# Optimization experiments

Measured on AMD Instinct MI355X. Metric: run time of the kernel, lower is better.

The kernel has to match this reference:

```python
import jax, jax.numpy as jnp
import numpy as np

B, N, D = 4, 4096, 1024
H = 16
DH = D // H  # 64
SCALE = DH ** 0.5


def setup_inputs() -> dict:
    key = jax.random.key(0)
    ks = jax.random.split(key, 10)
    bound = float(np.sqrt(6.0 / (D + D)))  # xavier_uniform for square weights
    lin_b = float(1.0 / np.sqrt(D))        # default nn.Linear bias init bound
    return {
        "q": jax.random.normal(ks[0], (B, N, D), dtype=jnp.float32),
        "k": jax.random.normal(ks[1], (B, N, D), dtype=jnp.float32),
        "v": jax.random.normal(ks[2], (B, N, D), dtype=jnp.float32),
        "Wq": jax.random.uniform(ks[3], (D, D), jnp.float32, -bound, bound),
        "bq": jax.random.uniform(ks[4], (D,), jnp.float32, -lin_b, lin_b),
        "Wk": jax.random.uniform(ks[5], (D, D), jnp.float32, -bound, bound),
        "bk": jax.random.uniform(ks[6], (D,), jnp.float32, -lin_b, lin_b),
        "Wv": jax.random.uniform(ks[7], (D, D), jnp.float32, -bound, bound),
        "bv": jax.random.uniform(ks[8], (D,), jnp.float32, -lin_b, lin_b),
        "Wo": jax.random.uniform(ks[9], (D, D), jnp.float32, -bound, bound),
    }


def _split_heads(x):
    # [b, n, h*d] -> [b, h, n, d]
    b, n, _ = x.shape
    return x.reshape(b, n, H, DH).transpose(0, 2, 1, 3)


def reference(q, k, v, Wq, bq, Wk, bk, Wv, bv, Wo):
    qp = _split_heads(q @ Wq.T + bq)  # [b,h,n,d]
    kp = _split_heads(k @ Wk.T + bk)
    vp = _split_heads(v @ Wv.T + bv)

    inv_qtr = SCALE ** (-0.25)
    qs = jax.nn.softmax(qp, axis=-1) * inv_qtr            # feature-wise softmax on Q
    ctx = jnp.einsum('bhnd,bhne->bhde', kp, vp)           # K^T V: [b,h,d,d]
    ctx = jax.nn.softmax(ctx, axis=-2) * inv_qtr          # softmax over first d axis
    att = jnp.einsum('bhnd,bhde->bhne', qs, ctx)          # [b,h,n,d]

    att = att.transpose(0, 2, 1, 3).reshape(q.shape[0], q.shape[1], D)  # b n (h d)
    return att @ Wo.T  # to_out linear (no bias); dropout p=0 -> identity
```

## Files before the change

### kernel.cpp

```cpp
#include <hip/hip_runtime.h>

#define INV_QTR 0.59460355750136053f

typedef _Float16 f16;
typedef _Float16 f16x8 __attribute__((ext_vector_type(8)));
typedef float f32x4 __attribute__((ext_vector_type(4)));

__device__ __forceinline__ void gload16(const void* g, void* l) {
    __builtin_amdgcn_global_load_lds(
        (const __attribute__((address_space(1))) void*)g,
        (__attribute__((address_space(3))) void*)l, 16, 0, 0);
}

template <bool OF, bool BIAS, bool QSM>
__device__ __forceinline__ void gemm_f16_body(const f16* __restrict__ X,
                                              const f16* __restrict__ W,
                                              const float* __restrict__ bias,
                                              void* __restrict__ dst) {
    __shared__ __align__(16) f16 As[128 * 64];
    __shared__ __align__(16) f16 Bs[128 * 64];

    const int tid  = threadIdx.x;
    const int lane = tid & 63;
    const int wave = tid >> 6;
    const int m0   = blockIdx.x * 128;
    const int n0   = blockIdx.y * 128;
    const int wm   = (wave >> 1) * 64;
    const int wn   = (wave & 1) * 64;
    const int frow = lane & 15;
    const int quad = lane >> 4;

    f32x4 acc[4][4] = {};

    for (int k0 = 0; k0 < 1024; k0 += 64) {
        __syncthreads();
        #pragma unroll
        for (int i = 0; i < 4; ++i) {
            int slot = i * 256 + tid;
            int row  = slot >> 3;
            int sc   = slot & 7;
            int gc   = sc ^ (row & 7);
            gload16(X + (size_t)(m0 + row) * 1024 + k0 + gc * 8,
                    (char*)As + slot * 16);
            gload16(W + (size_t)(n0 + row) * 1024 + k0 + gc * 8,
                    (char*)Bs + slot * 16);
        }
        __syncthreads();

        #pragma unroll
        for (int kk = 0; kk < 2; ++kk) {
            f16x8 fa[4], fb[4];
            #pragma unroll
            for (int t = 0; t < 4; ++t) {
                int arow = wm + t * 16 + frow;
                int asc  = (kk * 4 + quad) ^ (arow & 7);
                fa[t] = *(const f16x8*)(As + arow * 64 + asc * 8);
                int brow = wn + t * 16 + frow;
                int bsc  = (kk * 4 + quad) ^ (brow & 7);
                fb[t] = *(const f16x8*)(Bs + brow * 64 + bsc * 8);
            }
            #pragma unroll
            for (int tm = 0; tm < 4; ++tm)
                #pragma unroll
                for (int tn = 0; tn < 4; ++tn)
                    acc[tm][tn] = __builtin_amdgcn_mfma_f32_16x16x32_f16(
                        fa[tm], fb[tn], acc[tm][tn], 0, 0, 0);
        }
    }

    if (QSM) {
        float badd[4];
        #pragma unroll
        for (int tn = 0; tn < 4; ++tn) badd[tn] = bias[n0 + wn + tn * 16 + frow];
        #pragma unroll
        for (int tm = 0; tm < 4; ++tm) {
            #pragma unroll
            for (int r = 0; r < 4; ++r) {
                float x[4], m = -1e30f;
                #pragma unroll
                for (int tn = 0; tn < 4; ++tn) {
                    x[tn] = acc[tm][tn][r] + badd[tn];
                    m = fmaxf(m, x[tn]);
                }
                #pragma unroll
                for (int s = 1; s < 16; s <<= 1) m = fmaxf(m, __shfl_xor(m, s, 64));
                float e[4], sum = 0.f;
                #pragma unroll
                for (int tn = 0; tn < 4; ++tn) { e[tn] = __expf(x[tn] - m); sum += e[tn]; }
                #pragma unroll
                for (int s = 1; s < 16; s <<= 1) sum += __shfl_xor(sum, s, 64);
                float inv = INV_QTR / sum;
                size_t rowb = (size_t)(m0 + wm + tm * 16 + quad * 4 + r) * 1024;
                #pragma unroll
                for (int tn = 0; tn < 4; ++tn)
                    ((f16*)dst)[rowb + n0 + wn + tn * 16 + frow] = (f16)(e[tn] * inv);
            }
        }
        return;
    }

    #pragma unroll
    for (int tn = 0; tn < 4; ++tn) {
        int col = n0 + wn + tn * 16 + frow;
        float badd = BIAS ? bias[col] : 0.0f;
        #pragma unroll
        for (int tm = 0; tm < 4; ++tm) {
            #pragma unroll
            for (int r = 0; r < 4; ++r) {
                size_t idx = (size_t)(m0 + wm + tm * 16 + quad * 4 + r) * 1024 + col;
                float v = acc[tm][tn][r] + badd;
                if (OF) ((float*)dst)[idx] = v;
                else    ((f16*)dst)[idx] = (f16)v;
            }
        }
    }
}

__global__ void proj_qsm_gemm(const f16* __restrict__ X, const f16* __restrict__ W,
                              const float* __restrict__ bias, f16* __restrict__ dst) {
    gemm_f16_body<false, true, true>(X, W, bias, dst);
}

__global__ void out_gemm(const f16* __restrict__ att, const f16* __restrict__ Wo,
                         float* __restrict__ out) {
    gemm_f16_body<true, false, false>(att, Wo, nullptr, out);
}

template <int MODE, bool CS>
__global__ void transpose_cvt(const float* __restrict__ src, f16* __restrict__ dst0,
                              f16* __restrict__ dst1, float* __restrict__ csum) {
    __shared__ float T[64][65];
    int n0 = blockIdx.x * 64, c0 = blockIdx.y * 64, b = blockIdx.z;
    int tid = threadIdx.x;
    const float* s = src + ((size_t)b * 4096 + n0) * 1024 + c0;
    int r = tid >> 2, q4 = tid & 3;
    #pragma unroll
    for (int i = 0; i < 4; ++i) {
        f32x4 v = *(const f32x4*)(s + (size_t)r * 1024 + q4 * 16 + i * 4);
        #pragma unroll
        for (int j = 0; j < 4; ++j) T[q4 * 16 + i * 4 + j][r] = v[j];
    }
    __syncthreads();
    int cc = tid >> 2, nq = tid & 3;
    size_t obase = ((size_t)b * 1024 + c0 + cc) * 4096 + n0 + nq * 16;
    float x[16];
    #pragma unroll
    for (int j = 0; j < 16; ++j) x[j] = T[cc][nq * 16 + j];
    if (CS) {
        float ssum = 0.f;
        #pragma unroll
        for (int j = 0; j < 16; ++j) ssum += x[j];
        ssum += __shfl_xor(ssum, 1, 64);
        ssum += __shfl_xor(ssum, 2, 64);
        if (nq == 0) atomicAdd(csum + b * 1024 + c0 + cc, ssum);
    }
    f16x8 hi0, hi1;
    #pragma unroll
    for (int j = 0; j < 8; ++j) { hi0[j] = (f16)x[j]; hi1[j] = (f16)x[8 + j]; }
    if (MODE == 0 || MODE == 1) {
        *(f16x8*)(dst0 + obase) = hi0;
        *(f16x8*)(dst0 + obase + 8) = hi1;
    }
    if (MODE == 0 || MODE == 2) {
        f16x8 lo0, lo1;
        #pragma unroll
        for (int j = 0; j < 8; ++j) {
            lo0[j] = (f16)(x[j] - (float)hi0[j]);
            lo1[j] = (f16)(x[8 + j] - (float)hi1[j]);
        }
        f16* d = (MODE == 0) ? dst1 : dst0;
        *(f16x8*)(d + obase) = lo0;
        *(f16x8*)(d + obase + 8) = lo1;
    }
}

template <int NB, bool ACCUM>
__global__ void gram_gemm(const f16* __restrict__ A, const f16* __restrict__ B0,
                          const f16* __restrict__ B1, float* __restrict__ G0,
                          float* __restrict__ G1) {
    __shared__ __align__(16) f16 As[128 * 64];
    __shared__ __align__(16) f16 Bs0[128 * 64];
    __shared__ __align__(16) f16 Bs1[NB == 2 ? 128 * 64 : 8];
    const int tid = threadIdx.x, lane = tid & 63, wave = tid >> 6;
    const int zsel = blockIdx.x;
    const int m0 = blockIdx.y * 128, n0 = blockIdx.z * 128;
    const int b = zsel >> 1, kh = zsel & 1;
    const int wm = (wave >> 1) * 64, wn = (wave & 1) * 64;
    const int frow = lane & 15, quad = lane >> 4;
    const f16* Ab  = A + (size_t)b * 4194304;
    const f16* B0b = B0 + (size_t)b * 4194304;
    const f16* B1b = (NB == 2) ? B1 + (size_t)b * 4194304 : nullptr;
    float* Gd = (kh ? G1 : G0) + (size_t)b * 1048576;
    const int kbase = kh * 2048;
    f32x4 acc[4][4] = {};

    for (int k0 = kbase; k0 < kbase + 2048; k0 += 64) {
        __syncthreads();
        #pragma unroll
        for (int i = 0; i < 4; ++i) {
            int slot = i * 256 + tid, row = slot >> 3, sc = slot & 7;
            int gc = sc ^ (row & 7);
            gload16(Ab + (size_t)(m0 + row) * 4096 + k0 + gc * 8, (char*)As + slot * 16);
            gload16(B0b + (size_t)(n0 + row) * 4096 + k0 + gc * 8, (char*)Bs0 + slot * 16);
            if (NB == 2)
                gload16(B1b + (size_t)(n0 + row) * 4096 + k0 + gc * 8, (char*)Bs1 + slot * 16);
        }
        __syncthreads();
        #pragma unroll
        for (int kk = 0; kk < 2; ++kk) {
            f16x8 fa[4], fb0[4], fb1[4];
            #pragma unroll
            for (int t = 0; t < 4; ++t) {
                int arow = wm + t * 16 + frow;
                int asc  = (kk * 4 + quad) ^ (arow & 7);
                fa[t] = *(const f16x8*)(As + arow * 64 + asc * 8);
                int brow = wn + t * 16 + frow;
                int bsc  = (kk * 4 + quad) ^ (brow & 7);
                fb0[t] = *(const f16x8*)(Bs0 + brow * 64 + bsc * 8);
                if (NB == 2) fb1[t] = *(const f16x8*)(Bs1 + brow * 64 + bsc * 8);
            }
            #pragma unroll
            for (int tm = 0; tm < 4; ++tm)
                #pragma unroll
                for (int tn = 0; tn < 4; ++tn) {
                    acc[tm][tn] = __builtin_amdgcn_mfma_f32_16x16x32_f16(
                        fa[tm], fb0[tn], acc[tm][tn], 0, 0, 0);
                    if (NB == 2)
                        acc[tm][tn] = __builtin_amdgcn_mfma_f32_16x16x32_f16(
                            fa[tm], fb1[tn], acc[tm][tn], 0, 0, 0);
                }
        }
    }
    #pragma unroll
    for (int tn = 0; tn < 4; ++tn) {
        int col = n0 + wn + tn * 16 + frow;
        #pragma unroll
        for (int tm = 0; tm < 4; ++tm)
            #pragma unroll
            for (int r = 0; r < 4; ++r) {
                size_t idx = (size_t)(m0 + wm + tm * 16 + quad * 4 + r) * 1024 + col;
                if (ACCUM) Gd[idx] += acc[tm][tn][r];
                else       Gd[idx]  = acc[tm][tn][r];
            }
    }
}

__global__ void combine_split(const float* __restrict__ a, const float* __restrict__ b,
                              f16* __restrict__ hi, f16* __restrict__ lo) {
    size_t i = ((size_t)blockIdx.x * 256 + threadIdx.x) * 8;
    f32x4 a0 = *(const f32x4*)(a + i);
    f32x4 a1 = *(const f32x4*)(a + i + 4);
    f32x4 b0 = *(const f32x4*)(b + i);
    f32x4 b1 = *(const f32x4*)(b + i + 4);
    f16x8 h, l;
    #pragma unroll
    for (int j = 0; j < 4; ++j) {
        float s0 = a0[j] + b0[j], s1 = a1[j] + b1[j];
        h[j] = (f16)s0;     l[j] = (f16)(s0 - (float)h[j]);
        h[4 + j] = (f16)s1; l[4 + j] = (f16)(s1 - (float)h[4 + j]);
    }
    *(f16x8*)(hi + i) = h;
    *(f16x8*)(lo + i) = l;
}

__global__ void a3f16_gemm(const f16* __restrict__ wkhi, const f16* __restrict__ wklo,
                           const f16* __restrict__ ghi, const f16* __restrict__ glo,
                           float* __restrict__ P0, float* __restrict__ P1) {
    __shared__ __align__(16) f16 As0[128 * 64], As1[128 * 64];
    __shared__ __align__(16) f16 Bs0[128 * 64], Bs1[128 * 64];
    const int tid = threadIdx.x, lane = tid & 63, wave = tid >> 6;
    const int zsel = blockIdx.x;
    const int m0 = blockIdx.y * 128, n0 = blockIdx.z * 128;
    const int b = zsel >> 1, kh = zsel & 1;
    const int wm = (wave >> 1) * 64, wn = (wave & 1) * 64;
    const int frow = lane & 15, quad = lane >> 4;
    const f16* g0b = ghi + (size_t)b * 1048576;
    const f16* g1b = glo + (size_t)b * 1048576;
    float* Pd = (kh ? P1 : P0) + (size_t)b * 1048576;
    const int kbase = kh * 512;
    f32x4 acc[4][4] = {};

    for (int k0 = kbase; k0 < kbase + 512; k0 += 64) {
        __syncthreads();
        #pragma unroll
        for (int i = 0; i < 4; ++i) {
            int slot = i * 256 + tid, row = slot >> 3, sc = slot & 7;
            int gc = sc ^ (row & 7);
            size_t ao = (size_t)(m0 + row) * 1024 + k0 + gc * 8;
            size_t bo = (size_t)(n0 + row) * 1024 + k0 + gc * 8;
            gload16(wkhi + ao, (char*)As0 + slot * 16);
            gload16(wklo + ao, (char*)As1 + slot * 16);
            gload16(g0b + bo, (char*)Bs0 + slot * 16);
            gload16(g1b + bo, (char*)Bs1 + slot * 16);
        }
        __syncthreads();
        #pragma unroll
        for (int kk = 0; kk < 2; ++kk) {
            f16x8 fa0[4], fa1[4], fb0[4], fb1[4];
            #pragma unroll
            for (int t = 0; t < 4; ++t) {
                int arow = wm + t * 16 + frow;
                int asc  = (kk * 4 + quad) ^ (arow & 7);
                fa0[t] = *(const f16x8*)(As0 + arow * 64 + asc * 8);
                fa1[t] = *(const f16x8*)(As1 + arow * 64 + asc * 8);
                int brow = wn + t * 16 + frow;
                int bsc  = (kk * 4 + quad) ^ (brow & 7);
                fb0[t] = *(const f16x8*)(Bs0 + brow * 64 + bsc * 8);
                fb1[t] = *(const f16x8*)(Bs1 + brow * 64 + bsc * 8);
            }
            #pragma unroll
            for (int tm = 0; tm < 4; ++tm)
                #pragma unroll
                for (int tn = 0; tn < 4; ++tn) {
                    acc[tm][tn] = __builtin_amdgcn_mfma_f32_16x16x32_f16(
                        fa0[tm], fb0[tn], acc[tm][tn], 0, 0, 0);
                    acc[tm][tn] = __builtin_amdgcn_mfma_f32_16x16x32_f16(
                        fa1[tm], fb0[tn], acc[tm][tn], 0, 0, 0);
                    acc[tm][tn] = __builtin_amdgcn_mfma_f32_16x16x32_f16(
                        fa0[tm], fb1[tn], acc[tm][tn], 0, 0, 0);
                }
        }
    }
    #pragma unroll
    for (int tn = 0; tn < 4; ++tn) {
        int col = n0 + wn + tn * 16 + frow;
        #pragma unroll
        for (int tm = 0; tm < 4; ++tm)
            #pragma unroll
            for (int r = 0; r < 4; ++r)
                Pd[(size_t)(m0 + wm + tm * 16 + quad * 4 + r) * 1024 + col] =
                    acc[tm][tn][r];
    }
}

__global__ void zero_f32(float* __restrict__ p) {
    size_t i = ((size_t)blockIdx.x * 256 + threadIdx.x) * 4;
    *(f32x4*)(p + i) = f32x4{0.f, 0.f, 0.f, 0.f};
}

__global__ void bias_vec(const float* __restrict__ sk, const float* __restrict__ sv,
                         const float* __restrict__ Wk, const float* __restrict__ Wv,
                         float* __restrict__ u, float* __restrict__ w) {
    int gid = blockIdx.x * 4 + (threadIdx.x >> 6);
    int lane = threadIdx.x & 63;
    int b = gid >> 10, d = gid & 1023;
    const float* W = blockIdx.y ? Wv : Wk;
    const float* s = blockIdx.y ? sv : sk;
    float* dst = blockIdx.y ? w : u;
    const float* wr = W + (size_t)d * 1024;
    const float* sr = s + b * 1024;
    float acc = 0.f;
    #pragma unroll
    for (int t = 0; t < 16; ++t) acc += wr[lane + t * 64] * sr[lane + t * 64];
    #pragma unroll
    for (int s2 = 32; s2; s2 >>= 1) acc += __shfl_xor(acc, s2, 64);
    if (lane == 0) dst[b * 1024 + d] = acc;
}

__global__ void ctx_gemm_softmax(const f16* __restrict__ a3hi, const f16* __restrict__ a3lo,
                                 const f16* __restrict__ wvhi, const f16* __restrict__ wvlo,
                                 const float* __restrict__ u, const float* __restrict__ wvec,
                                 const float* __restrict__ bk, const float* __restrict__ bv,
                                 f16* __restrict__ ctxT) {
    __shared__ __align__(16) f16 As0[64 * 64], As1[64 * 64], Bs0[64 * 64], Bs1[64 * 64];
    __shared__ float cs[64 * 65];
    int bh = blockIdx.x, b = bh >> 4, h = bh & 15;
    int tid = threadIdx.x, lane = tid & 63, wave = tid >> 6;
    const size_t abase = (size_t)b * 1048576 + (size_t)(h * 64) * 1024;
    const size_t wbase = (size_t)(h * 64) * 1024;
    int frow = lane & 15, quad = lane >> 4;
    f32x4 acc[4] = {};

    for (int k0 = 0; k0 < 1024; k0 += 64) {
        __syncthreads();
        #pragma unroll
        for (int i = 0; i < 2; ++i) {
            int slot = i * 256 + tid, row = slot >> 3, sc = slot & 7;
            int gc = sc ^ (row & 7);
            size_t ro = (size_t)row * 1024 + k0 + gc * 8;
            gload16(a3hi + abase + ro, (char*)As0 + slot * 16);
            gload16(a3lo + abase + ro, (char*)As1 + slot * 16);
            gload16(wvhi + wbase + ro, (char*)Bs0 + slot * 16);
            gload16(wvlo + wbase + ro, (char*)Bs1 + slot * 16);
        }
        __syncthreads();
        #pragma unroll
        for (int kk = 0; kk < 2; ++kk) {
            int arow = wave * 16 + frow;
            int asc  = (kk * 4 + quad) ^ (arow & 7);
            f16x8 fa0 = *(const f16x8*)(As0 + arow * 64 + asc * 8);
            f16x8 fa1 = *(const f16x8*)(As1 + arow * 64 + asc * 8);
            #pragma unroll
            for (int tn = 0; tn < 4; ++tn) {
                int brow = tn * 16 + frow;
                int bsc  = (kk * 4 + quad) ^ (brow & 7);
                f16x8 fb0 = *(const f16x8*)(Bs0 + brow * 64 + bsc * 8);
                f16x8 fb1 = *(const f16x8*)(Bs1 + brow * 64 + bsc * 8);
                acc[tn] = __builtin_amdgcn_mfma_f32_16x16x32_f16(fa0, fb0, acc[tn], 0, 0, 0);
                acc[tn] = __builtin_amdgcn_mfma_f32_16x16x32_f16(fa1, fb0, acc[tn], 0, 0, 0);
                acc[tn] = __builtin_amdgcn_mfma_f32_16x16x32_f16(fa0, fb1, acc[tn], 0, 0, 0);
            }
        }
    }

    const float* ub  = u + b * 1024 + h * 64;
    const float* wb  = wvec + b * 1024 + h * 64;
    const float* bkh = bk + h * 64;
    const float* bvh = bv + h * 64;
    #pragma unroll
    for (int tn = 0; tn < 4; ++tn) {
        int ee = tn * 16 + frow;
        float bve = bvh[ee], we = wb[ee];
        #pragma unroll
        for (int r = 0; r < 4; ++r) {
            int dd = wave * 16 + quad * 4 + r;
            float bkd = bkh[dd], ud = ub[dd];
            cs[dd * 65 + ee] = acc[tn][r] + bkd * we + bve * ud + 4096.0f * bkd * bve;
        }
    }
    __syncthreads();
    #pragma unroll
    for (int i = 0; i < 16; ++i) {
        int e = wave * 16 + i;
        float x = cs[lane * 65 + e];
        float m = x;
        #pragma unroll
        for (int s2 = 32; s2; s2 >>= 1) m = fmaxf(m, __shfl_xor(m, s2, 64));
        float ex = __expf(x - m);
        float sum = ex;
        #pragma unroll
        for (int s2 = 32; s2; s2 >>= 1) sum += __shfl_xor(sum, s2, 64);
        ctxT[((size_t)bh * 64 + e) * 64 + lane] = (f16)(ex / sum * INV_QTR);
    }
}

__global__ void att_gemm(const f16* __restrict__ qs, const f16* __restrict__ ctxT,
                         f16* __restrict__ att) {
    __shared__ __align__(16) f16 As[2][128 * 64];
    __shared__ __align__(16) f16 Bs[2][64 * 64];
    int tid = threadIdx.x, lane = tid & 63, wave = tid >> 6;
    int m0 = blockIdx.x * 128;
    int n0 = blockIdx.y * 128;
    int b  = m0 >> 12;
    int h0 = (n0 >> 6) & 15;

    #pragma unroll
    for (int ch = 0; ch < 2; ++ch) {
        #pragma unroll
        for (int i = 0; i < 4; ++i) {
            int slot = i * 256 + tid, row = slot >> 3, sc = slot & 7, gc = sc ^ (row & 7);
            gload16(qs + (size_t)(m0 + row) * 1024 + n0 + ch * 64 + gc * 8,
                    (char*)As[ch] + slot * 16);
        }
        #pragma unroll
        for (int i = 0; i < 2; ++i) {
            int slot = i * 256 + tid, row = slot >> 3, sc = slot & 7, gc = sc ^ (row & 7);
            int bh = b * 16 + h0 + ch;
            gload16(ctxT + ((size_t)bh * 64 + row) * 64 + gc * 8,
                    (char*)Bs[ch] + slot * 16);
        }
    }
    __syncthreads();

    int wm = (wave >> 1) * 64, wn = wave & 1;
    int frow = lane & 15, quad = lane >> 4;
    f32x4 acc[4][4] = {};
    #pragma unroll
    for (int kk = 0; kk < 2; ++kk) {
        f16x8 fa[4], fb[4];
        #pragma unroll
        for (int t = 0; t < 4; ++t) {
            int arow = wm + t * 16 + frow;
            int asc  = (kk * 4 + quad) ^ (arow & 7);
            fa[t] = *(const f16x8*)(As[wn] + arow * 64 + asc * 8);
            int brow = t * 16 + frow;
            int bsc  = (kk * 4 + quad) ^ (brow & 7);
            fb[t] = *(const f16x8*)(Bs[wn] + brow * 64 + bsc * 8);
        }
        #pragma unroll
        for (int tm = 0; tm < 4; ++tm)
            #pragma unroll
            for (int tn = 0; tn < 4; ++tn)
                acc[tm][tn] = __builtin_amdgcn_mfma_f32_16x16x32_f16(
                    fa[tm], fb[tn], acc[tm][tn], 0, 0, 0);
    }
    #pragma unroll
    for (int tn = 0; tn < 4; ++tn) {
        int col = n0 + wn * 64 + tn * 16 + frow;
        #pragma unroll
        for (int tm = 0; tm < 4; ++tm) {
            #pragma unroll
            for (int r = 0; r < 4; ++r) {
                int row = m0 + wm + tm * 16 + quad * 4 + r;
                att[(size_t)row * 1024 + col] = (f16)acc[tm][tn][r];
            }
        }
    }
}

__device__ __forceinline__ void cvt8_hilo(const float* src, f16* dh, f16* dl, bool lo) {
    f32x4 a = ((const f32x4*)src)[0];
    f32x4 b = ((const f32x4*)src)[1];
    f16x8 h, l;
    #pragma unroll
    for (int j = 0; j < 4; ++j) {
        h[j] = (f16)a[j];     h[j + 4] = (f16)b[j];
        l[j] = (f16)(a[j] - (float)h[j]);
        l[j + 4] = (f16)(b[j] - (float)h[j + 4]);
    }
    *(f16x8*)dh = h;
    if (lo) *(f16x8*)dl = l;
}

__global__ void cvt_w_kv(const float* __restrict__ Wk, const float* __restrict__ Wv,
                         f16* __restrict__ whik, f16* __restrict__ whiv,
                         f16* __restrict__ wlok, f16* __restrict__ wlov) {
    const float* s = blockIdx.y ? Wv : Wk;
    f16* dh = blockIdx.y ? whiv : whik;
    f16* dl = blockIdx.y ? wlov : wlok;
    size_t i = ((size_t)blockIdx.x * 256 + threadIdx.x) * 8;
    cvt8_hilo(s + i, dh + i, dl + i, true);
}

__global__ void cvt_q_wqo(const float* __restrict__ q, const float* __restrict__ Wq,
                          const float* __restrict__ Wo, f16* __restrict__ qh,
                          f16* __restrict__ wqhi, f16* __restrict__ wohi) {
    size_t i = ((size_t)blockIdx.x * 256 + threadIdx.x) * 8;
    const float* src;
    f16* dst;
    if (i < 16777216) { src = q + i; dst = qh + i; }
    else {
        size_t wi = i - 16777216;
        if (wi < 1048576) { src = Wq + wi; dst = wqhi + wi; }
        else              { src = Wo + (wi - 1048576); dst = wohi + (wi - 1048576); }
    }
    cvt8_hilo(src, dst, nullptr, false);
}

extern "C" void kernel_launch(void* const* d_in, const int* in_sizes, int n_in,
                              void* d_out, int out_size, void* d_ws, size_t ws_size,
                              hipStream_t stream) {
    const float* q  = (const float*)d_in[0];
    const float* k  = (const float*)d_in[1];
    const float* v  = (const float*)d_in[2];
    const float* Wq = (const float*)d_in[3];
    const float* bq = (const float*)d_in[4];
    const float* Wk = (const float*)d_in[5];
    const float* bk = (const float*)d_in[6];
    const float* Wv = (const float*)d_in[7];
    const float* bv = (const float*)d_in[8];
    const float* Wo = (const float*)d_in[9];

    const size_t Mi = 1048576;
    char* ws = (char*)d_ws;
    char* ob = (char*)d_out;

    f16*   Ghi  = (f16*)ws;
    f16*   Glo  = (f16*)(ws + 8 * Mi);
    f16*   A3hi = (f16*)(ws + 16 * Mi);
    f16*   A3lo = (f16*)(ws + 24 * Mi);
    float* G0   = (float*)(ws + 32 * Mi);
    float* G1   = (float*)(ws + 48 * Mi);
    f16*   Wkhi = (f16*)(ws + 64 * Mi);
    f16*   Wvhi = (f16*)(ws + 66 * Mi);
    f16*   Wklo = (f16*)(ws + 68 * Mi);
    f16*   Wvlo = (f16*)(ws + 70 * Mi);
    f16*   ctxT = (f16*)(ws + 72 * Mi);
    float* sk   = (float*)(ws + 72 * Mi + 524288);
    float* sv   = (float*)(ws + 72 * Mi + 540672);
    float* u    = (float*)(ws + 72 * Mi + 557056);
    float* w    = (float*)(ws + 72 * Mi + 573440);
    f16*   XvTh = (f16*)ws;
    f16*   Wqhi = (f16*)(ws + 32 * Mi);
    f16*   Wohi = (f16*)(ws + 34 * Mi);
    f16*   att  = (f16*)(ws + 36 * Mi);

    f16*   XkTh = (f16*)ob;
    f16*   XkTl = (f16*)(ob + 32 * Mi);
    f16*   XvTl = (f16*)(ob + 32 * Mi);
    float* P0   = (float*)ob;
    float* P1   = (float*)(ob + 16 * Mi);
    f16*   qh   = (f16*)ob;
    f16*   qp   = (f16*)(ob + 32 * Mi);
    float* out  = (float*)d_out;

    zero_f32<<<8, 256, 0, stream>>>(sk);
    cvt_w_kv<<<dim3(512, 2), 256, 0, stream>>>(Wk, Wv, Wkhi, Wvhi, Wklo, Wvlo);
    transpose_cvt<0, true><<<dim3(64, 16, 4), 256, 0, stream>>>(k, XkTh, XkTl, sk);
    transpose_cvt<1, true><<<dim3(64, 16, 4), 256, 0, stream>>>(v, XvTh, nullptr, sv);
    gram_gemm<2, false><<<dim3(8, 8, 8), 256, 0, stream>>>(XvTh, XkTh, XkTl, G0, G1);
    transpose_cvt<2, false><<<dim3(64, 16, 4), 256, 0, stream>>>(v, XvTl, nullptr, nullptr);
    gram_gemm<1, true><<<dim3(8, 8, 8), 256, 0, stream>>>(XvTl, XkTh, nullptr, G0, G1);
    combine_split<<<2048, 256, 0, stream>>>(G0, G1, Ghi, Glo);
    a3f16_gemm<<<dim3(8, 8, 8), 256, 0, stream>>>(Wkhi, Wklo, Ghi, Glo, P0, P1);
    combine_split<<<2048, 256, 0, stream>>>(P0, P1, A3hi, A3lo);
    bias_vec<<<dim3(1024, 2), 256, 0, stream>>>(sk, sv, Wk, Wv, u, w);
    ctx_gemm_softmax<<<64, 256, 0, stream>>>(A3hi, A3lo, Wvhi, Wvlo, u, w, bk, bv, ctxT);
    cvt_q_wqo<<<9216, 256, 0, stream>>>(q, Wq, Wo, qh, Wqhi, Wohi);
    proj_qsm_gemm<<<dim3(128, 8), 256, 0, stream>>>(qh, Wqhi, bq, qp);
    att_gemm<<<dim3(128, 8), 256, 0, stream>>>(qp, ctxT, att);
    out_gemm<<<dim3(128, 8), 256, 0, stream>>>(att, Wohi, out);
}
```

Baseline: 597.1 us.

## Fuse Q projection softmax with attention GEMM and merge small prep kernels

Fuses the Q projection, its feature-wise softmax, and the qs·ctx product into one kernel that keeps the softmaxed tile in shared memory, so the qp intermediate is never written to or read from global memory. It also merges the weight conversion with the K/V transposes, and the bias-vector computation with the G combine. The column sums now use per-block partial writes plus a reduction in place of atomics and a zeroing kernel. The P0+P1 combine and hi/lo split is folded into the ctx kernel's tile loads. Together these cut launch count and intermediate global traffic, at the cost of more shared memory per block and register pressure in the fused kernel.

```diff
diff --git a/kernel.cpp b/kernel.cpp
--- a/kernel.cpp
+++ b/kernel.cpp
@@ -12,7 +12,7 @@
         (__attribute__((address_space(3))) void*)l, 16, 0, 0);
 }
 
-template <bool OF, bool BIAS, bool QSM>
+template <bool OF, bool BIAS>
 __device__ __forceinline__ void gemm_f16_body(const f16* __restrict__ X,
                                               const f16* __restrict__ W,
                                               const float* __restrict__ bias,
@@ -68,37 +68,6 @@
         }
     }
 
-    if (QSM) {
-        float badd[4];
-        #pragma unroll
-        for (int tn = 0; tn < 4; ++tn) badd[tn] = bias[n0 + wn + tn * 16 + frow];
-        #pragma unroll
-        for (int tm = 0; tm < 4; ++tm) {
-            #pragma unroll
-            for (int r = 0; r < 4; ++r) {
-                float x[4], m = -1e30f;
-                #pragma unroll
-                for (int tn = 0; tn < 4; ++tn) {
-                    x[tn] = acc[tm][tn][r] + badd[tn];
-                    m = fmaxf(m, x[tn]);
-                }
-                #pragma unroll
-                for (int s = 1; s < 16; s <<= 1) m = fmaxf(m, __shfl_xor(m, s, 64));
-                float e[4], sum = 0.f;
-                #pragma unroll
-                for (int tn = 0; tn < 4; ++tn) { e[tn] = __expf(x[tn] - m); sum += e[tn]; }
-                #pragma unroll
-                for (int s = 1; s < 16; s <<= 1) sum += __shfl_xor(sum, s, 64);
-                float inv = INV_QTR / sum;
-                size_t rowb = (size_t)(m0 + wm + tm * 16 + quad * 4 + r) * 1024;
-                #pragma unroll
-                for (int tn = 0; tn < 4; ++tn)
-                    ((f16*)dst)[rowb + n0 + wn + tn * 16 + frow] = (f16)(e[tn] * inv);
-            }
-        }
-        return;
-    }
-
     #pragma unroll
     for (int tn = 0; tn < 4; ++tn) {
         int col = n0 + wn + tn * 16 + frow;
@@ -116,21 +85,19 @@
     }
 }
 
-__global__ void proj_qsm_gemm(const f16* __restrict__ X, const f16* __restrict__ W,
-                              const float* __restrict__ bias, f16* __restrict__ dst) {
-    gemm_f16_body<false, true, true>(X, W, bias, dst);
-}
-
 __global__ void out_gemm(const f16* __restrict__ att, const f16* __restrict__ Wo,
                          float* __restrict__ out) {
-    gemm_f16_body<true, false, false>(att, Wo, nullptr, out);
+    gemm_f16_body<true, false>(att, Wo, nullptr, out);
 }
 
 template <int MODE, bool CS>
-__global__ void transpose_cvt(const float* __restrict__ src, f16* __restrict__ dst0,
-                              f16* __restrict__ dst1, float* __restrict__ csum) {
-    __shared__ float T[64][65];
-    int n0 = blockIdx.x * 64, c0 = blockIdx.y * 64, b = blockIdx.z;
+__device__ __forceinline__ void transpose_body(const float* __restrict__ src,
+                                               f16* __restrict__ dst0,
+                                               f16* __restrict__ dst1,
+                                               float* __restrict__ csum,
+                                               int bx, int by, int bz,
+                                               float (*T)[65]) {
+    int n0 = bx * 64, c0 = by * 64, b = bz;
     int tid = threadIdx.x;
     const float* s = src + ((size_t)b * 4096 + n0) * 1024 + c0;
     int r = tid >> 2, q4 = tid & 3;
@@ -152,7 +119,7 @@
         for (int j = 0; j < 16; ++j) ssum += x[j];
         ssum += __shfl_xor(ssum, 1, 64);
         ssum += __shfl_xor(ssum, 2, 64);
-        if (nq == 0) atomicAdd(csum + b * 1024 + c0 + cc, ssum);
+        if (nq == 0) csum[((size_t)(b * 1024 + c0 + cc)) * 64 + bx] = ssum;
     }
     f16x8 hi0, hi1;
     #pragma unroll
@@ -171,6 +138,66 @@
         f16* d = (MODE == 0) ? dst1 : dst0;
         *(f16x8*)(d + obase) = lo0;
         *(f16x8*)(d + obase + 8) = lo1;
+    }
+}
+
+__device__ __forceinline__ void cvt8_hilo(const float* src, f16* dh, f16* dl, bool lo) {
+    f32x4 a = ((const f32x4*)src)[0];
+    f32x4 b = ((const f32x4*)src)[1];
+    f16x8 h, l;
+    #pragma unroll
+    for (int j = 0; j < 4; ++j) {
+        h[j] = (f16)a[j];     h[j + 4] = (f16)b[j];
+        l[j] = (f16)(a[j] - (float)h[j]);
+        l[j + 4] = (f16)(b[j] - (float)h[j + 4]);
+    }
+    *(f16x8*)dh = h;
+    if (lo) *(f16x8*)dl = l;
+}
+
+__global__ void prep_kernel(const float* __restrict__ k, const float* __restrict__ v,
+                            const float* __restrict__ Wk, const float* __restrict__ Wv,
+                            f16* __restrict__ XkTh, f16* __restrict__ XkTl,
+                            f16* __restrict__ XvTh,
+                            f16* __restrict__ whik, f16* __restrict__ whiv,
+                            f16* __restrict__ wlok, f16* __restrict__ wlov,
+                            float* __restrict__ pk, float* __restrict__ pv) {
+    __shared__ float T[64][65];
+    int bid = blockIdx.x;
+    if (bid < 4096) {
+        transpose_body<0, true>(k, XkTh, XkTl, pk, bid & 63, (bid >> 6) & 15,
+                                bid >> 10, T);
+    } else if (bid < 8192) {
+        int g = bid - 4096;
+        transpose_body<1, true>(v, XvTh, nullptr, pv, g & 63, (g >> 6) & 15,
+                                g >> 10, T);
+    } else {
+        int g = bid - 8192;
+        const float* s = (g >= 512) ? Wv : Wk;
+        f16* dh = (g >= 512) ? whiv : whik;
+        f16* dl = (g >= 512) ? wlov : wlok;
+        size_t i = ((size_t)(g & 511) * 256 + threadIdx.x) * 8;
+        cvt8_hilo(s + i, dh + i, dl + i, true);
+    }
+}
+
+__global__ void tvlo_kernel(const float* __restrict__ v, f16* __restrict__ XvTl,
+                            const float* __restrict__ pk, const float* __restrict__ pv,
+                            float* __restrict__ sk, float* __restrict__ sv) {
+    __shared__ float T[64][65];
+    int bid = blockIdx.x;
+    if (bid < 4096) {
+        transpose_body<2, false>(v, XvTl, nullptr, nullptr, bid & 63,
+                                 (bid >> 6) & 15, bid >> 10, T);
+    } else {
+        int idx = (bid - 4096) * 256 + threadIdx.x;
+        const float* p = (idx < 4096) ? pk : pv;
+        float* d = (idx < 4096) ? sk : sv;
+        int c = idx & 4095;
+        float s = 0.f;
+        #pragma unroll
+        for (int ch = 0; ch < 64; ++ch) s += p[(size_t)c * 64 + ch];
+        d[c] = s;
     }
 }
 
@@ -245,22 +272,45 @@
     }
 }
 
-__global__ void combine_split(const float* __restrict__ a, const float* __restrict__ b,
-                              f16* __restrict__ hi, f16* __restrict__ lo) {
-    size_t i = ((size_t)blockIdx.x * 256 + threadIdx.x) * 8;
-    f32x4 a0 = *(const f32x4*)(a + i);
-    f32x4 a1 = *(const f32x4*)(a + i + 4);
-    f32x4 b0 = *(const f32x4*)(b + i);
-    f32x4 b1 = *(const f32x4*)(b + i + 4);
-    f16x8 h, l;
-    #pragma unroll
-    for (int j = 0; j < 4; ++j) {
-        float s0 = a0[j] + b0[j], s1 = a1[j] + b1[j];
-        h[j] = (f16)s0;     l[j] = (f16)(s0 - (float)h[j]);
-        h[4 + j] = (f16)s1; l[4 + j] = (f16)(s1 - (float)h[4 + j]);
-    }
-    *(f16x8*)(hi + i) = h;
-    *(f16x8*)(lo + i) = l;
+__global__ void mid_kernel(const float* __restrict__ G0, const float* __restrict__ G1,
+                           f16* __restrict__ Ghi, f16* __restrict__ Glo,
+                           const float* __restrict__ sk, const float* __restrict__ sv,
+                           const float* __restrict__ Wk, const float* __restrict__ Wv,
+                           float* __restrict__ u, float* __restrict__ w) {
+    int bid = blockIdx.x;
+    if (bid < 2048) {
+        size_t i = ((size_t)bid * 256 + threadIdx.x) * 8;
+        f32x4 a0 = *(const f32x4*)(G0 + i);
+        f32x4 a1 = *(const f32x4*)(G0 + i + 4);
+        f32x4 b0 = *(const f32x4*)(G1 + i);
+        f32x4 b1 = *(const f32x4*)(G1 + i + 4);
+        f16x8 h, l;
+        #pragma unroll
+        for (int j = 0; j < 4; ++j) {
+            float s0 = a0[j] + b0[j], s1 = a1[j] + b1[j];
+            h[j] = (f16)s0;     l[j] = (f16)(s0 - (float)h[j]);
+            h[4 + j] = (f16)s1; l[4 + j] = (f16)(s1 - (float)h[4 + j]);
+        }
+        *(f16x8*)(Ghi + i) = h;
+        *(f16x8*)(Glo + i) = l;
+    } else {
+        int g = bid - 2048;
+        int yy = g >> 10;
+        int gid = (g & 1023) * 4 + (threadIdx.x >> 6);
+        int lane = threadIdx.x & 63;
+        int b = gid >> 10, d = gid & 1023;
+        const float* W = yy ? Wv : Wk;
+        const float* s = yy ? sv : sk;
+        float* dst = yy ? w : u;
+        const float* wr = W + (size_t)d * 1024;
+        const float* sr = s + b * 1024;
+        float acc = 0.f;
+        #pragma unroll
+        for (int t = 0; t < 16; ++t) acc += wr[lane + t * 64] * sr[lane + t * 64];
+        #pragma unroll
+        for (int s2 = 32; s2; s2 >>= 1) acc += __shfl_xor(acc, s2, 64);
+        if (lane == 0) dst[b * 1024 + d] = acc;
+    }
 }
 
 __global__ void a3f16_gemm(const f16* __restrict__ wkhi, const f16* __restrict__ wklo,
@@ -333,40 +383,17 @@
     }
 }
 
-__global__ void zero_f32(float* __restrict__ p) {
-    size_t i = ((size_t)blockIdx.x * 256 + threadIdx.x) * 4;
-    *(f32x4*)(p + i) = f32x4{0.f, 0.f, 0.f, 0.f};
-}
-
-__global__ void bias_vec(const float* __restrict__ sk, const float* __restrict__ sv,
-                         const float* __restrict__ Wk, const float* __restrict__ Wv,
-                         float* __restrict__ u, float* __restrict__ w) {
-    int gid = blockIdx.x * 4 + (threadIdx.x >> 6);
-    int lane = threadIdx.x & 63;
-    int b = gid >> 10, d = gid & 1023;
-    const float* W = blockIdx.y ? Wv : Wk;
-    const float* s = blockIdx.y ? sv : sk;
-    float* dst = blockIdx.y ? w : u;
-    const float* wr = W + (size_t)d * 1024;
-    const float* sr = s + b * 1024;
-    float acc = 0.f;
-    #pragma unroll
-    for (int t = 0; t < 16; ++t) acc += wr[lane + t * 64] * sr[lane + t * 64];
-    #pragma unroll
-    for (int s2 = 32; s2; s2 >>= 1) acc += __shfl_xor(acc, s2, 64);
-    if (lane == 0) dst[b * 1024 + d] = acc;
-}
-
-__global__ void ctx_gemm_softmax(const f16* __restrict__ a3hi, const f16* __restrict__ a3lo,
-                                 const f16* __restrict__ wvhi, const f16* __restrict__ wvlo,
-                                 const float* __restrict__ u, const float* __restrict__ wvec,
-                                 const float* __restrict__ bk, const float* __restrict__ bv,
-                                 f16* __restrict__ ctxT) {
+__global__ void ctx_ps(const float* __restrict__ P0, const float* __restrict__ P1,
+                       const f16* __restrict__ wvhi, const f16* __restrict__ wvlo,
+                       const float* __restrict__ u, const float* __restrict__ wvec,
+                       const float* __restrict__ bk, const float* __restrict__ bv,
+                       f16* __restrict__ ctxT) {
     __shared__ __align__(16) f16 As0[64 * 64], As1[64 * 64], Bs0[64 * 64], Bs1[64 * 64];
     __shared__ float cs[64 * 65];
     int bh = blockIdx.x, b = bh >> 4, h = bh & 15;
     int tid = threadIdx.x, lane = tid & 63, wave = tid >> 6;
-    const size_t abase = (size_t)b * 1048576 + (size_t)(h * 64) * 1024;
+    const float* p0b = P0 + (size_t)b * 1048576 + (size_t)(h * 64) * 1024;
+    const float* p1b = P1 + (size_t)b * 1048576 + (size_t)(h * 64) * 1024;
     const size_t wbase = (size_t)(h * 64) * 1024;
     int frow = lane & 15, quad = lane >> 4;
     f32x4 acc[4] = {};
@@ -378,8 +405,19 @@
             int slot = i * 256 + tid, row = slot >> 3, sc = slot & 7;
             int gc = sc ^ (row & 7);
             size_t ro = (size_t)row * 1024 + k0 + gc * 8;
-            gload16(a3hi + abase + ro, (char*)As0 + slot * 16);
-            gload16(a3lo + abase + ro, (char*)As1 + slot * 16);
+            f32x4 xa = *(const f32x4*)(p0b + ro);
+            f32x4 xb = *(const f32x4*)(p0b + ro + 4);
+            f32x4 ya = *(const f32x4*)(p1b + ro);
+            f32x4 yb = *(const f32x4*)(p1b + ro + 4);
+            f16x8 hh, ll;
+            #pragma unroll
+            for (int j = 0; j < 4; ++j) {
+                float s0 = xa[j] + ya[j], s1 = xb[j] + yb[j];
+                hh[j] = (f16)s0;     ll[j] = (f16)(s0 - (float)hh[j]);
+                hh[4 + j] = (f16)s1; ll[4 + j] = (f16)(s1 - (float)hh[4 + j]);
+            }
+            *(f16x8*)((char*)As0 + slot * 16) = hh;
+            *(f16x8*)((char*)As1 + slot * 16) = ll;
             gload16(wvhi + wbase + ro, (char*)Bs0 + slot * 16);
             gload16(wvlo + wbase + ro, (char*)Bs1 + slot * 16);
         }
@@ -432,94 +470,6 @@
         for (int s2 = 32; s2; s2 >>= 1) sum += __shfl_xor(sum, s2, 64);
         ctxT[((size_t)bh * 64 + e) * 64 + lane] = (f16)(ex / sum * INV_QTR);
     }
-}
-
-__global__ void att_gemm(const f16* __restrict__ qs, const f16* __restrict__ ctxT,
-                         f16* __restrict__ att) {
-    __shared__ __align__(16) f16 As[2][128 * 64];
-    __shared__ __align__(16) f16 Bs[2][64 * 64];
-    int tid = threadIdx.x, lane = tid & 63, wave = tid >> 6;
-    int m0 = blockIdx.x * 128;
-    int n0 = blockIdx.y * 128;
-    int b  = m0 >> 12;
-    int h0 = (n0 >> 6) & 15;
-
-    #pragma unroll
-    for (int ch = 0; ch < 2; ++ch) {
-        #pragma unroll
-        for (int i = 0; i < 4; ++i) {
-            int slot = i * 256 + tid, row = slot >> 3, sc = slot & 7, gc = sc ^ (row & 7);
-            gload16(qs + (size_t)(m0 + row) * 1024 + n0 + ch * 64 + gc * 8,
-                    (char*)As[ch] + slot * 16);
-        }
-        #pragma unroll
-        for (int i = 0; i < 2; ++i) {
-            int slot = i * 256 + tid, row = slot >> 3, sc = slot & 7, gc = sc ^ (row & 7);
-            int bh = b * 16 + h0 + ch;
-            gload16(ctxT + ((size_t)bh * 64 + row) * 64 + gc * 8,
-                    (char*)Bs[ch] + slot * 16);
-        }
-    }
-    __syncthreads();
-
-    int wm = (wave >> 1) * 64, wn = wave & 1;
-    int frow = lane & 15, quad = lane >> 4;
-    f32x4 acc[4][4] = {};
-    #pragma unroll
-    for (int kk = 0; kk < 2; ++kk) {
-        f16x8 fa[4], fb[4];
-        #pragma unroll
-        for (int t = 0; t < 4; ++t) {
-            int arow = wm + t * 16 + frow;
-            int asc  = (kk * 4 + quad) ^ (arow & 7);
-            fa[t] = *(const f16x8*)(As[wn] + arow * 64 + asc * 8);
-            int brow = t * 16 + frow;
-            int bsc  = (kk * 4 + quad) ^ (brow & 7);
-            fb[t] = *(const f16x8*)(Bs[wn] + brow * 64 + bsc * 8);
-        }
-        #pragma unroll
-        for (int tm = 0; tm < 4; ++tm)
-            #pragma unroll
-            for (int tn = 0; tn < 4; ++tn)
-                acc[tm][tn] = __builtin_amdgcn_mfma_f32_16x16x32_f16(
-                    fa[tm], fb[tn], acc[tm][tn], 0, 0, 0);
-    }
-    #pragma unroll
-    for (int tn = 0; tn < 4; ++tn) {
-        int col = n0 + wn * 64 + tn * 16 + frow;
-        #pragma unroll
-        for (int tm = 0; tm < 4; ++tm) {
-            #pragma unroll
-            for (int r = 0; r < 4; ++r) {
-                int row = m0 + wm + tm * 16 + quad * 4 + r;
-                att[(size_t)row * 1024 + col] = (f16)acc[tm][tn][r];
-            }
-        }
-    }
-}
-
-__device__ __forceinline__ void cvt8_hilo(const float* src, f16* dh, f16* dl, bool lo) {
-    f32x4 a = ((const f32x4*)src)[0];
-    f32x4 b = ((const f32x4*)src)[1];
-    f16x8 h, l;
-    #pragma unroll
-    for (int j = 0; j < 4; ++j) {
-        h[j] = (f16)a[j];     h[j + 4] = (f16)b[j];
-        l[j] = (f16)(a[j] - (float)h[j]);
-        l[j + 4] = (f16)(b[j] - (float)h[j + 4]);
-    }
-    *(f16x8*)dh = h;
-    if (lo) *(f16x8*)dl = l;
-}
-
-__global__ void cvt_w_kv(const float* __restrict__ Wk, const float* __restrict__ Wv,
-                         f16* __restrict__ whik, f16* __restrict__ whiv,
-                         f16* __restrict__ wlok, f16* __restrict__ wlov) {
-    const float* s = blockIdx.y ? Wv : Wk;
-    f16* dh = blockIdx.y ? whiv : whik;
-    f16* dl = blockIdx.y ? wlov : wlok;
-    size_t i = ((size_t)blockIdx.x * 256 + threadIdx.x) * 8;
-    cvt8_hilo(s + i, dh + i, dl + i, true);
 }
 
 __global__ void cvt_q_wqo(const float* __restrict__ q, const float* __restrict__ Wq,
@@ -535,6 +485,136 @@
         else              { src = Wo + (wi - 1048576); dst = wohi + (wi - 1048576); }
     }
     cvt8_hilo(src, dst, nullptr, false);
+}
+
+__global__ void __launch_bounds__(256)
+proj_att(const f16* __restrict__ qh, const f16* __restrict__ Wqhi,
+         const float* __restrict__ bias, const f16* __restrict__ ctxT,
+         f16* __restrict__ att) {
+    __shared__ __align__(16) char SMEM[34816];
+    __shared__ __align__(16) f16 ctxS[2][4096];
+    f16* As  = (f16*)SMEM;
+    f16* Bs  = (f16*)(SMEM + 16384);
+    f16* qsS = (f16*)SMEM;
+
+    const int tid  = threadIdx.x;
+    const int lane = tid & 63;
+    const int wave = tid >> 6;
+    const int m0   = blockIdx.x * 128;
+    const int n0   = blockIdx.y * 128;
+    const int wm   = (wave >> 1) * 64;
+    const int wn   = (wave & 1) * 64;
+    const int frow = lane & 15;
+    const int quad = lane >> 4;
+    const int b    = m0 >> 12;
+    const int h0   = (n0 >> 6) & 15;
+
+    #pragma unroll
+    for (int ch = 0; ch < 2; ++ch)
+        #pragma unroll
+        for (int i = 0; i < 2; ++i) {
+            int slot = i * 256 + tid, row = slot >> 3, gc = (slot & 7) ^ (row & 7);
+            int bh = b * 16 + h0 + ch;
+            gload16(ctxT + ((size_t)bh * 64 + row) * 64 + gc * 8,
+                    (char*)ctxS[ch] + slot * 16);
+        }
+
+    f32x4 acc[4][4] = {};
+    for (int k0 = 0; k0 < 1024; k0 += 64) {
+        __syncthreads();
+        #pragma unroll
+        for (int i = 0; i < 4; ++i) {
+            int slot = i * 256 + tid, row = slot >> 3, sc = slot & 7;
+            int gc = sc ^ (row & 7);
+            gload16(qh + (size_t)(m0 + row) * 1024 + k0 + gc * 8,
+                    (char*)As + slot * 16);
+            gload16(Wqhi + (size_t)(n0 + row) * 1024 + k0 + gc * 8,
+                    (char*)Bs + slot * 16);
+        }
+        __syncthreads();
+        #pragma unroll
+        for (int kk = 0; kk < 2; ++kk) {
+            f16x8 fa[4], fb[4];
+            #pragma unroll
+            for (int t = 0; t < 4; ++t) {
+                int arow = wm + t * 16 + frow;
+                int asc  = (kk * 4 + quad) ^ (arow & 7);
+                fa[t] = *(const f16x8*)(As + arow * 64 + asc * 8);
+                int brow = wn + t * 16 + frow;
+                int bsc  = (kk * 4 + quad) ^ (brow & 7);
+                fb[t] = *(const f16x8*)(Bs + brow * 64 + bsc * 8);
+            }
+            #pragma unroll
+            for (int tm = 0; tm < 4; ++tm)
+                #pragma unroll
+                for (int tn = 0; tn < 4; ++tn)
+                    acc[tm][tn] = __builtin_amdgcn_mfma_f32_16x16x32_f16(
+                        fa[tm], fb[tn], acc[tm][tn], 0, 0, 0);
+        }
+    }
+    __syncthreads();
+
+    float badd[4];
+    #pragma unroll
+    for (int tn = 0; tn < 4; ++tn) badd[tn] = bias[n0 + wn + tn * 16 + frow];
+    #pragma unroll
+    for (int tm = 0; tm < 4; ++tm) {
+        #pragma unroll
+        for (int r = 0; r < 4; ++r) {
+            float x[4], m = -1e30f;
+            #pragma unroll
+            for (int tn = 0; tn < 4; ++tn) {
+                x[tn] = acc[tm][tn][r] + badd[tn];
+                m = fmaxf(m, x[tn]);
+            }
+            #pragma unroll
+            for (int s = 1; s < 16; s <<= 1) m = fmaxf(m, __shfl_xor(m, s, 64));
+            float e[4], sum = 0.f;
+            #pragma unroll
+            for (int tn = 0; tn < 4; ++tn) { e[tn] = __expf(x[tn] - m); sum += e[tn]; }
+            #pragma unroll
+            for (int s = 1; s < 16; s <<= 1) sum += __shfl_xor(sum, s, 64);
+            float inv = INV_QTR / sum;
+            int lrow = wm + tm * 16 + quad * 4 + r;
+            #pragma unroll
+            for (int tn = 0; tn < 4; ++tn)
+                qsS[lrow * 136 + wn + tn * 16 + frow] = (f16)(e[tn] * inv);
+        }
+    }
+    __syncthreads();
+
+    f32x4 a2[4][4] = {};
+    const int chh = wave & 1;
+    #pragma unroll
+    for (int kk = 0; kk < 2; ++kk) {
+        f16x8 fa[4], fb[4];
+        #pragma unroll
+        for (int t = 0; t < 4; ++t) {
+            int arow = wm + t * 16 + frow;
+            fa[t] = *(const f16x8*)(qsS + arow * 136 + wn + (kk * 4 + quad) * 8);
+            int brow = t * 16 + frow;
+            int bsc  = (kk * 4 + quad) ^ (brow & 7);
+            fb[t] = *(const f16x8*)(ctxS[chh] + brow * 64 + bsc * 8);
+        }
+        #pragma unroll
+        for (int tm = 0; tm < 4; ++tm)
+            #pragma unroll
+            for (int tn = 0; tn < 4; ++tn)
+                a2[tm][tn] = __builtin_amdgcn_mfma_f32_16x16x32_f16(
+                    fa[tm], fb[tn], a2[tm][tn], 0, 0, 0);
+    }
+    #pragma unroll
+    for (int tn = 0; tn < 4; ++tn) {
+        int col = n0 + wn + tn * 16 + frow;
+        #pragma unroll
+        for (int tm = 0; tm < 4; ++tm) {
+            #pragma unroll
+            for (int r = 0; r < 4; ++r) {
+                int row = m0 + wm + tm * 16 + quad * 4 + r;
+                att[(size_t)row * 1024 + col] = (f16)a2[tm][tn][r];
+            }
+        }
+    }
 }
 
 extern "C" void kernel_launch(void* const* d_in, const int* in_sizes, int n_in,
@@ -557,8 +637,6 @@
 
     f16*   Ghi  = (f16*)ws;
     f16*   Glo  = (f16*)(ws + 8 * Mi);
-    f16*   A3hi = (f16*)(ws + 16 * Mi);
-    f16*   A3lo = (f16*)(ws + 24 * Mi);
     float* G0   = (float*)(ws + 32 * Mi);
     float* G1   = (float*)(ws + 48 * Mi);
     f16*   Wkhi = (f16*)(ws + 64 * Mi);
@@ -566,10 +644,12 @@
     f16*   Wklo = (f16*)(ws + 68 * Mi);
     f16*   Wvlo = (f16*)(ws + 70 * Mi);
     f16*   ctxT = (f16*)(ws + 72 * Mi);
-    float* sk   = (float*)(ws + 72 * Mi + 524288);
-    float* sv   = (float*)(ws + 72 * Mi + 540672);
-    float* u    = (float*)(ws + 72 * Mi + 557056);
-    float* w    = (float*)(ws + 72 * Mi + 573440);
+    float* pk   = (float*)(ws + 72 * Mi + 524288);
+    float* pv   = (float*)(ws + 72 * Mi + 1572864);
+    float* sk   = (float*)(ws + 72 * Mi + 2621440);
+    float* sv   = (float*)(ws + 72 * Mi + 2637824);
+    float* u    = (float*)(ws + 72 * Mi + 2654208);
+    float* w    = (float*)(ws + 72 * Mi + 2670592);
     f16*   XvTh = (f16*)ws;
     f16*   Wqhi = (f16*)(ws + 32 * Mi);
     f16*   Wohi = (f16*)(ws + 34 * Mi);
@@ -581,23 +661,17 @@
     float* P0   = (float*)ob;
     float* P1   = (float*)(ob + 16 * Mi);
     f16*   qh   = (f16*)ob;
-    f16*   qp   = (f16*)(ob + 32 * Mi);
     float* out  = (float*)d_out;
 
-    zero_f32<<<8, 256, 0, stream>>>(sk);
-    cvt_w_kv<<<dim3(512, 2), 256, 0, stream>>>(Wk, Wv, Wkhi, Wvhi, Wklo, Wvlo);
-    transpose_cvt<0, true><<<dim3(64, 16, 4), 256, 0, stream>>>(k, XkTh, XkTl, sk);
-    transpose_cvt<1, true><<<dim3(64, 16, 4), 256, 0, stream>>>(v, XvTh, nullptr, sv);
+    prep_kernel<<<9216, 256, 0, stream>>>(k, v, Wk, Wv, XkTh, XkTl, XvTh,
+                                          Wkhi, Wvhi, Wklo, Wvlo, pk, pv);
     gram_gemm<2, false><<<dim3(8, 8, 8), 256, 0, stream>>>(XvTh, XkTh, XkTl, G0, G1);
-    transpose_cvt<2, false><<<dim3(64, 16, 4), 256, 0, stream>>>(v, XvTl, nullptr, nullptr);
+    tvlo_kernel<<<4128, 256, 0, stream>>>(v, XvTl, pk, pv, sk, sv);
     gram_gemm<1, true><<<dim3(8, 8, 8), 256, 0, stream>>>(XvTl, XkTh, nullptr, G0, G1);
-    combine_split<<<2048, 256, 0, stream>>>(G0, G1, Ghi, Glo);
+    mid_kernel<<<4096, 256, 0, stream>>>(G0, G1, Ghi, Glo, sk, sv, Wk, Wv, u, w);
     a3f16_gemm<<<dim3(8, 8, 8), 256, 0, stream>>>(Wkhi, Wklo, Ghi, Glo, P0, P1);
-    combine_split<<<2048, 256, 0, stream>>>(P0, P1, A3hi, A3lo);
-    bias_vec<<<dim3(1024, 2), 256, 0, stream>>>(sk, sv, Wk, Wv, u, w);
-    ctx_gemm_softmax<<<64, 256, 0, stream>>>(A3hi, A3lo, Wvhi, Wvlo, u, w, bk, bv, ctxT);
+    ctx_ps<<<64, 256, 0, stream>>>(P0, P1, Wvhi, Wvlo, u, w, bk, bv, ctxT);
     cvt_q_wqo<<<9216, 256, 0, stream>>>(q, Wq, Wo, qh, Wqhi, Wohi);
-    proj_qsm_gemm<<<dim3(128, 8), 256, 0, stream>>>(qh, Wqhi, bq, qp);
-    att_gemm<<<dim3(128, 8), 256, 0, stream>>>(qp, ctxT, att);
+    proj_att<<<dim3(128, 8), 256, 0, stream>>>(qh, Wqhi, bq, ctxT, att);
     out_gemm<<<dim3(128, 8), 256, 0, stream>>>(att, Wohi, out);
 }
```

After: 597.0 us. No clear change (-0.0%).
